# Optimization experiments

Hardware: AMD Instinct MI355X
Metric: run time of the kernel (lower is better)

The kernel has to match this reference:

```python
import jax, jax.numpy as jnp
from jax import lax
import numpy as np

OBS_DIM, POP_DIM, ACT_DIM, DE_POP = 256, 10, 8, 10
HID1, HID2 = 256, 256
SPIKE_TS = 25
ENC_VTH = 0.999
CDECAY = 0.5
VDECAY = 0.75
VTH_TEMPORAL = 0.5  # NEURON_VTH_*_temporal stays at its init value 0.5
GRAD_WIN = 0.5


@jax.custom_vjp
def enc_spike(v):
    return (v > ENC_VTH).astype(v.dtype)

def _es_fwd(v):
    return enc_spike(v), None

def _es_bwd(_, g):
    return (g,)  # straight-through

enc_spike.defvjp(_es_fwd, _es_bwd)


@jax.custom_vjp
def rect_spike(v, vth):
    return (v > vth).astype(v.dtype)

def _rs_fwd(v, vth):
    return rect_spike(v, vth), (v, vth)

def _rs_bwd(res, g):
    v, vth = res
    # rectangular pseudo-gradient window; vth is detached in the original (numpy roundtrip)
    return (g * (jnp.abs(v - vth) < GRAD_WIN).astype(g.dtype), jnp.zeros_like(vth))

rect_spike.defvjp(_rs_fwd, _rs_bwd)


def setup_inputs() -> dict:
    key = jax.random.key(0)
    ks = jax.random.split(key, 10)
    B = 2048
    obs = jax.random.normal(ks[0], (B, OBS_DIM), dtype=jnp.float32)
    # encoder Gaussian receptive-field params
    enc_mean = jnp.broadcast_to(jnp.linspace(-3.0, 3.0, POP_DIM, dtype=jnp.float32), (1, OBS_DIM, POP_DIM))
    enc_std = jnp.full((1, OBS_DIM, POP_DIM), 0.15, dtype=jnp.float32)
    n_in = OBS_DIM * POP_DIM
    out_pop = ACT_DIM * DE_POP
    w1 = jax.random.normal(ks[1], (HID1, n_in), dtype=jnp.float32) / np.sqrt(n_in)
    b1 = jnp.zeros((HID1,), dtype=jnp.float32)
    w2 = jax.random.normal(ks[2], (HID2, HID1), dtype=jnp.float32) / np.sqrt(HID1)
    b2 = jnp.zeros((HID2,), dtype=jnp.float32)
    w3 = jax.random.normal(ks[3], (out_pop, HID2), dtype=jnp.float32) / np.sqrt(HID2)
    b3 = jnp.zeros((out_pop,), dtype=jnp.float32)
    dec_w = jax.random.normal(ks[4], (ACT_DIM, DE_POP), dtype=jnp.float32) / np.sqrt(DE_POP)
    dec_b = jnp.zeros((ACT_DIM,), dtype=jnp.float32)
    return {"obs": obs, "enc_mean": enc_mean, "enc_std": enc_std,
            "w1": w1, "b1": b1, "w2": w2, "b2": b2, "w3": w3, "b3": b3,
            "dec_w": dec_w, "dec_b": dec_b, "batch_size": B}


def _forward(obs, enc_mean, enc_std, w1, b1, w2, b2, w3, b3, dec_w, dec_b):
    B = obs.shape[0]
    # --- population encoder: Gaussian receptive fields -> regular spike train ---
    pop_act = jnp.exp(-0.5 * (obs[:, :, None] - enc_mean) ** 2 / (enc_std ** 2))
    pop_act = pop_act.reshape(B, OBS_DIM * POP_DIM)  # [B, N]

    def enc_step(volt, _):
        volt = volt + pop_act
        s = enc_spike(volt)
        return volt - s * ENC_VTH, s

    _, in_spikes = lax.scan(enc_step, jnp.zeros_like(pop_act), None, length=SPIKE_TS)  # [T, B, N]

    # --- spike MLP with LIF neurons and dynamic threshold ---
    def lif_dth(x, W, b, state):
        c, v_prev, s = state
        c = c * CDECAY + x @ W.T + b
        v = v_prev * VDECAY * (1.0 - s) + c
        # dynamic threshold (detached in original via numpy roundtrip)
        vth = lax.stop_gradient(0.5 * VTH_TEMPORAL + 0.5 * (jnp.exp((v_prev - v) / 3.0) - 1.0))
        s = rect_spike(v, vth)
        return (c, v, s)

    def zeros_state(n):
        z = jnp.zeros((B, n), dtype=obs.dtype)
        return (z, z, z)

    init = (zeros_state(HID1), zeros_state(HID2), zeros_state(ACT_DIM * DE_POP))

    def mlp_step(states, x):
        s1 = lif_dth(x, w1, b1, states[0])
        s2 = lif_dth(s1[2], w2, b2, states[1])
        s3 = lif_dth(s2[2], w3, b3, states[2])
        return (s1, s2, s3), s3[2]

    _, out_spikes = lax.scan(mlp_step, init, in_spikes)  # [T, B, out_pop]
    pop_out = out_spikes.sum(axis=0) / SPIKE_TS  # rate decode

    # --- decoder: grouped Conv1d(kernel=pop_dim) == per-action dot product, then tanh ---
    raw = jnp.einsum('bap,ap->ba', pop_out.reshape(B, ACT_DIM, DE_POP), dec_w) + dec_b
    return jnp.tanh(raw)


def reference(obs, enc_mean, enc_std, w1, b1, w2, b2, w3, b3, dec_w, dec_b, batch_size):
    return _forward(obs, enc_mean, enc_std, w1, b1, w2, b2, w3, b3, dec_w, dec_b)
```

## Files before the change

### kernel.cpp

```cpp
#include <hip/hip_runtime.h>
#include <stdint.h>

#define NB 2048
#define OBSD 256
#define POP 10
#define NIN 2560
#define H 256
#define OUTP 80
#define TS 25
#define CAP 256

typedef __attribute__((ext_vector_type(2))) float f2;

__device__ __forceinline__ float exp_cr(float x) {
    return (float)exp((double)x);
}

__device__ __forceinline__ int rfl(int v) {
    return __builtin_amdgcn_readfirstlane(v);
}

struct Acc25 {
    f2 p[12];
    float last;
};

__device__ __forceinline__ void acc_zero(Acc25& a) {
    #pragma unroll
    for (int i = 0; i < 12; ++i) { a.p[i].x = 0.0f; a.p[i].y = 0.0f; }
    a.last = 0.0f;
}

__device__ __forceinline__ void acc_fold(Acc25& acc, Acc25& part) {
    #pragma unroll
    for (int i = 0; i < 12; ++i) {
        acc.p[i].x = __fadd_rn(acc.p[i].x, part.p[i].x);
        acc.p[i].y = __fadd_rn(acc.p[i].y, part.p[i].y);
        part.p[i].x = 0.0f; part.p[i].y = 0.0f;
    }
    acc.last = __fadd_rn(acc.last, part.last);
    part.last = 0.0f;
}

__device__ __forceinline__ void acc_unpack(const Acc25& a, float* __restrict__ t) {
    #pragma unroll
    for (int i = 0; i < 12; ++i) { t[2 * i] = a.p[i].x; t[2 * i + 1] = a.p[i].y; }
    t[24] = a.last;
}

__device__ __forceinline__ void fma25(float w, const float* __restrict__ rec, float lastv, Acc25& a) {
    f2 wp; wp.x = w; wp.y = w;
    float4 q[6];
    #pragma unroll
    for (int i = 0; i < 6; ++i) q[i] = ((const float4*)rec)[i];
    const f2* r2 = (const f2*)q;
    #pragma unroll
    for (int i = 0; i < 12; ++i) {
#if __has_builtin(__builtin_elementwise_fma)
        a.p[i] = __builtin_elementwise_fma(wp, r2[i], a.p[i]);
#else
        a.p[i].x = fmaf(w, r2[i].x, a.p[i].x);
        a.p[i].y = fmaf(w, r2[i].y, a.p[i].y);
#endif
    }
    a.last = fmaf(w, lastv, a.last);
}

__device__ __forceinline__ void write_rec(float* __restrict__ recs, float* __restrict__ rec24,
                                          int pos, uint32_t m) {
    if (pos >= CAP) return;
    float f[24];
    #pragma unroll
    for (int t = 0; t < 24; ++t) f[t] = (m >> t) & 1u ? 1.0f : 0.0f;
    float4* dst = (float4*)&recs[pos * 24];
    #pragma unroll
    for (int p = 0; p < 6; ++p)
        dst[p] = make_float4(f[4 * p], f[4 * p + 1], f[4 * p + 2], f[4 * p + 3]);
    rec24[pos] = (m >> 24) & 1u ? 1.0f : 0.0f;
}

template<bool FOLD>
__device__ __forceinline__ void walk(int n, const float* __restrict__ wt, int tid,
        const int* __restrict__ idxL, const float* __restrict__ recs,
        const float* __restrict__ rec24, Acc25& acc, Acc25& part, int& nextB)
{
    Acc25& tgt = FOLD ? part : acc;
    int pi0 = 0, pi1 = 0, pi2 = 0, pi3 = 0;
    float pw0 = 0, pw1 = 0, pw2 = 0, pw3 = 0;
    if (n > 0) { pi0 = rfl(idxL[0]); pw0 = wt[pi0 + tid]; }
    if (n > 1) { pi1 = rfl(idxL[1]); pw1 = wt[pi1 + tid]; }
    if (n > 2) { pi2 = rfl(idxL[2]); pw2 = wt[pi2 + tid]; }
    if (n > 3) { pi3 = rfl(idxL[3]); pw3 = wt[pi3 + tid]; }
    int j = 0;
    for (; j + 4 <= n; j += 4) {
        int ci0 = pi0, ci1 = pi1, ci2 = pi2, ci3 = pi3;
        float cw0 = pw0, cw1 = pw1, cw2 = pw2, cw3 = pw3;
        if (j + 4 < n) { pi0 = rfl(idxL[j + 4]); pw0 = wt[pi0 + tid]; }
        if (j + 5 < n) { pi1 = rfl(idxL[j + 5]); pw1 = wt[pi1 + tid]; }
        if (j + 6 < n) { pi2 = rfl(idxL[j + 6]); pw2 = wt[pi2 + tid]; }
        if (j + 7 < n) { pi3 = rfl(idxL[j + 7]); pw3 = wt[pi3 + tid]; }
        if (FOLD) { while (ci0 >= nextB) { acc_fold(acc, part); nextB += 320 * H; } }
        fma25(cw0, recs + j * 24, rec24[j], tgt);
        if (FOLD) { while (ci1 >= nextB) { acc_fold(acc, part); nextB += 320 * H; } }
        fma25(cw1, recs + (j + 1) * 24, rec24[j + 1], tgt);
        if (FOLD) { while (ci2 >= nextB) { acc_fold(acc, part); nextB += 320 * H; } }
        fma25(cw2, recs + (j + 2) * 24, rec24[j + 2], tgt);
        if (FOLD) { while (ci3 >= nextB) { acc_fold(acc, part); nextB += 320 * H; } }
        fma25(cw3, recs + (j + 3) * 24, rec24[j + 3], tgt);
    }
    for (; j < n; ++j) {
        int ii = rfl(idxL[j]);
        float wv = wt[ii + tid];
        if (FOLD) { while (ii >= nextB) { acc_fold(acc, part); nextB += 320 * H; } }
        fma25(wv, recs + j * 24, rec24[j], tgt);
    }
}

__global__ __launch_bounds__(256) void k0_transpose(
    const float* __restrict__ w1, const float* __restrict__ w2, const float* __restrict__ w3,
    float* __restrict__ w1t, float* __restrict__ w2t, float* __restrict__ w3t)
{
    __shared__ float tile[32][33];
    int bid = blockIdx.x;
    const float* src; float* dst; int R, C, tr, tc;
    if (bid < 640)      { src = w1; dst = w1t; R = 256; C = NIN; tr = bid / 80; tc = bid % 80; }
    else if (bid < 704) { int t = bid - 640; src = w2; dst = w2t; R = 256; C = 256; tr = t / 8; tc = t % 8; }
    else                { int t = bid - 704; src = w3; dst = w3t; R = OUTP; C = 256; tr = t / 8; tc = t % 8; }
    const int tx = threadIdx.x & 31, ty = threadIdx.x >> 5;
    const int r0 = tr * 32, c0 = tc * 32;
    #pragma unroll
    for (int i = 0; i < 4; ++i) {
        int r = r0 + ty + i * 8, c = c0 + tx;
        if (r < R && c < C) tile[ty + i * 8][tx] = src[r * C + c];
    }
    __syncthreads();
    #pragma unroll
    for (int i = 0; i < 4; ++i) {
        int c = c0 + ty + i * 8, r = r0 + tx;
        if (c < C && r < R) dst[c * R + r] = tile[tx][ty + i * 8];
    }
}

__device__ __forceinline__ void lif_step(float x, float bv, float& c, float& v, float& s) {
    float cn = __fadd_rn(__fadd_rn(__fmul_rn(c, 0.5f), x), bv);
    c = cn;
    float vp = v;
    float t  = __fmul_rn(__fmul_rn(vp, 0.75f), __fadd_rn(1.0f, -s));
    float vn = __fadd_rn(t, cn);
    float ag = __fdiv_rn(__fadd_rn(vp, -vn), 3.0f);
    v = vn;
    float ex_a  = __expf(ag);
    float vth_a = 0.25f + 0.5f * (ex_a - 1.0f);
    float delta = 1e-5f * (ex_a + fabsf(vth_a) + 1.0f);
    if (vn > vth_a + delta) {
        s = 1.0f;
    } else if (vn < vth_a - delta) {
        s = 0.0f;
    } else {
        float ex  = exp_cr(ag);
        float vth = __fadd_rn(0.25f, __fmul_rn(0.5f, __fadd_rn(ex, -1.0f)));
        s = (vn > vth) ? 1.0f : 0.0f;
    }
}

__global__ __launch_bounds__(256, 6) void k1_fused(
    const float* __restrict__ obs, const float* __restrict__ emean, const float* __restrict__ estd,
    const float* __restrict__ w1t, const float* __restrict__ w2t, const float* __restrict__ w3t,
    const float* __restrict__ b1, const float* __restrict__ b2, const float* __restrict__ b3,
    const float* __restrict__ dw, const float* __restrict__ db, float* __restrict__ out)
{
    __shared__ __align__(16) float recs[CAP * 24];
    __shared__ float rec24[CAP];
    __shared__ int   idxL[CAP];
    __shared__ uint32_t cntA[40];
    __shared__ uint32_t waveCnt[4];
    __shared__ float cnt3[OUTP];

    const int tid = threadIdx.x;
    const int wave = tid >> 6, lane = tid & 63;
    const int b = blockIdx.x;
    const unsigned long long below = (1ull << lane) - 1ull;

    uint32_t msk[10];
    #pragma unroll
    for (int k = 0; k < 10; ++k) {
        int i = k * 256 + tid;
        int o = i / 10;
        float x  = obs[b * OBSD + o];
        float mu = emean[i];
        float sd = estd[i];
        float d  = __fadd_rn(x, -mu);
        float d2 = __fmul_rn(d, d);
        float nm = __fmul_rn(-0.5f, d2);
        float dn = __fmul_rn(sd, sd);
        float arg = __fdiv_rn(nm, dn);
        uint32_t m = 0;
        if (arg >= -3.23f) {
            float a  = exp_cr(arg);
            float volt = 0.0f;
            #pragma unroll
            for (int t = 0; t < TS; ++t) {
                volt = __fadd_rn(volt, a);
                if (volt > 0.999f) { m |= (1u << t); volt = __fadd_rn(volt, -0.999f); }
            }
        }
        msk[k] = m;
    }

    #pragma unroll
    for (int k = 0; k < 10; ++k) {
        unsigned long long bal = __ballot(msk[k] != 0u);
        if (lane == 0) cntA[k * 4 + wave] = (uint32_t)__popcll(bal);
    }
    __syncthreads();

    Acc25 acc, part;
    acc_zero(acc); acc_zero(part);
    int nextB = 320 * H;
    int run = 0;
    #pragma unroll
    for (int k = 0; k < 10; ++k) {
        if (k == 5) {
            __syncthreads();
            walk<true>(run, w1t, tid, idxL, recs, rec24, acc, part, nextB);
            __syncthreads();
            run = 0;
        }
        int tot = 0, pre = 0;
        #pragma unroll
        for (int w = 0; w < 4; ++w) {
            int c = (int)cntA[k * 4 + w];
            tot += c;
            if (w < wave) pre += c;
        }
        uint32_t m = msk[k];
        unsigned long long bal = __ballot(m != 0u);
        if (m) {
            int pos = run + pre + (int)__popcll(bal & below);
            idxL[pos] = (k * 256 + tid) * H;
            write_rec(recs, rec24, pos, m);
        }
        run += tot;
    }
    __syncthreads();
    walk<true>(run, w1t, tid, idxL, recs, rec24, acc, part, nextB);
    acc_fold(acc, part);

    uint32_t m1 = 0;
    {
        float cur[TS];
        acc_unpack(acc, cur);
        const float b1v = b1[tid];
        float c1 = 0, v1 = 0, s1 = 0;
        #pragma unroll
        for (int t = 0; t < TS; ++t) {
            lif_step(cur[t], b1v, c1, v1, s1);
            if (s1 != 0.0f) m1 |= (1u << t);
        }
    }
    unsigned long long bal1 = __ballot(m1 != 0u);
    if (lane == 0) waveCnt[wave] = (uint32_t)__popcll(bal1);
    __syncthreads();
    int base1 = 0, n1 = 0;
    #pragma unroll
    for (int w = 0; w < 4; ++w) {
        if (w < wave) base1 += (int)waveCnt[w];
        n1 += (int)waveCnt[w];
    }
    if (m1) {
        int pos = base1 + (int)__popcll(bal1 & below);
        idxL[pos] = tid * H;
        write_rec(recs, rec24, pos, m1);
    }
    __syncthreads();

    Acc25 acc2;
    acc_zero(acc2);
    {
        int dummyB = 0x7fffffff;
        walk<false>(n1, w2t, tid, idxL, recs, rec24, acc2, acc2, dummyB);
    }
    uint32_t m2 = 0;
    {
        float cur[TS];
        acc_unpack(acc2, cur);
        const float b2v = b2[tid];
        float c2 = 0, v2 = 0, s2 = 0;
        #pragma unroll
        for (int t = 0; t < TS; ++t) {
            lif_step(cur[t], b2v, c2, v2, s2);
            if (s2 != 0.0f) m2 |= (1u << t);
        }
    }
    unsigned long long bal2 = __ballot(m2 != 0u);
    if (lane == 0) waveCnt[wave] = (uint32_t)__popcll(bal2);
    __syncthreads();
    int base2 = 0, n2 = 0;
    #pragma unroll
    for (int w = 0; w < 4; ++w) {
        if (w < wave) base2 += (int)waveCnt[w];
        n2 += (int)waveCnt[w];
    }
    if (m2) {
        int pos = base2 + (int)__popcll(bal2 & below);
        idxL[pos] = tid * OUTP;
        write_rec(recs, rec24, pos, m2);
    }
    __syncthreads();

    if (tid < OUTP) {
        Acc25 x3;
        acc_zero(x3);
        int dummyB = 0x7fffffff;
        walk<false>(n2, w3t, tid, idxL, recs, rec24, x3, x3, dummyB);
        float cur[TS];
        acc_unpack(x3, cur);
        const float b3v = b3[tid];
        float c3 = 0, v3 = 0, s3 = 0, ct = 0;
        #pragma unroll
        for (int t = 0; t < TS; ++t) {
            lif_step(cur[t], b3v, c3, v3, s3);
            ct += s3;
        }
        cnt3[tid] = ct;
    }
    __syncthreads();

    if (tid < 8) {
        float raw = 0.0f;
        #pragma unroll
        for (int pp = 0; pp < POP; ++pp) {
            float po = __fdiv_rn(cnt3[tid * POP + pp], 25.0f);
            raw = __fadd_rn(raw, __fmul_rn(po, dw[tid * POP + pp]));
        }
        raw = __fadd_rn(raw, db[tid]);
        out[b * 8 + tid] = (float)tanh((double)raw);
    }
}

extern "C" void kernel_launch(void* const* d_in, const int* in_sizes, int n_in,
                              void* d_out, int out_size, void* d_ws, size_t ws_size,
                              hipStream_t stream) {
    const float* obs   = (const float*)d_in[0];
    const float* emean = (const float*)d_in[1];
    const float* estd  = (const float*)d_in[2];
    const float* w1    = (const float*)d_in[3];
    const float* b1    = (const float*)d_in[4];
    const float* w2    = (const float*)d_in[5];
    const float* b2    = (const float*)d_in[6];
    const float* w3    = (const float*)d_in[7];
    const float* b3    = (const float*)d_in[8];
    const float* dw    = (const float*)d_in[9];
    const float* db    = (const float*)d_in[10];
    float* out = (float*)d_out;

    char* ws = (char*)d_ws;
    float* w1t = (float*)(ws);
    float* w2t = (float*)(ws + 2621440);
    float* w3t = (float*)(ws + 2883584);

    k0_transpose<<<728, 256, 0, stream>>>(w1, w2, w3, w1t, w2t, w3t);
    k1_fused<<<NB, 256, 0, stream>>>(obs, emean, estd, w1t, w2t, w3t,
                                     b1, b2, b3, dw, db, out);
}
```

Baseline: 383.0 us.

## Shrink shared spike buffer with chunked walks and raise occupancy target

Cuts the shared spike-record capacity from 256 to 88 entries and processes every layer's active inputs in chunks of that size, each chunk bracketed by block barriers. Per-thread spike masks move to shared memory and per-group bases are prefix-summed once. The launch bound is raised to 8 blocks per CU and the weight walk is unrolled by 2 instead of 4. All of this aims to lower LDS and register use so more blocks fit per CU. The LIF step also swaps the divide by 3 for a reciprocal multiply and widens the fallback tolerance. The cost is extra barriers and chunk loops, plus less memory-level parallelism in the gather.

```diff
diff --git a/kernel.cpp b/kernel.cpp
--- a/kernel.cpp
+++ b/kernel.cpp
@@ -8,7 +8,7 @@
 #define H 256
 #define OUTP 80
 #define TS 25
-#define CAP 256
+#define CAP 88
 
 typedef __attribute__((ext_vector_type(2))) float f2;
 
@@ -68,7 +68,6 @@
 
 __device__ __forceinline__ void write_rec(float* __restrict__ recs, float* __restrict__ rec24,
                                           int pos, uint32_t m) {
-    if (pos >= CAP) return;
     float f[24];
     #pragma unroll
     for (int t = 0; t < 24; ++t) f[t] = (m >> t) & 1u ? 1.0f : 0.0f;
@@ -79,42 +78,28 @@
     rec24[pos] = (m >> 24) & 1u ? 1.0f : 0.0f;
 }
 
-template<bool FOLD>
-__device__ __forceinline__ void walk(int n, const float* __restrict__ wt, int tid,
-        const int* __restrict__ idxL, const float* __restrict__ recs,
-        const float* __restrict__ rec24, Acc25& acc, Acc25& part, int& nextB)
-{
-    Acc25& tgt = FOLD ? part : acc;
-    int pi0 = 0, pi1 = 0, pi2 = 0, pi3 = 0;
-    float pw0 = 0, pw1 = 0, pw2 = 0, pw3 = 0;
-    if (n > 0) { pi0 = rfl(idxL[0]); pw0 = wt[pi0 + tid]; }
-    if (n > 1) { pi1 = rfl(idxL[1]); pw1 = wt[pi1 + tid]; }
-    if (n > 2) { pi2 = rfl(idxL[2]); pw2 = wt[pi2 + tid]; }
-    if (n > 3) { pi3 = rfl(idxL[3]); pw3 = wt[pi3 + tid]; }
-    int j = 0;
-    for (; j + 4 <= n; j += 4) {
-        int ci0 = pi0, ci1 = pi1, ci2 = pi2, ci3 = pi3;
-        float cw0 = pw0, cw1 = pw1, cw2 = pw2, cw3 = pw3;
-        if (j + 4 < n) { pi0 = rfl(idxL[j + 4]); pw0 = wt[pi0 + tid]; }
-        if (j + 5 < n) { pi1 = rfl(idxL[j + 5]); pw1 = wt[pi1 + tid]; }
-        if (j + 6 < n) { pi2 = rfl(idxL[j + 6]); pw2 = wt[pi2 + tid]; }
-        if (j + 7 < n) { pi3 = rfl(idxL[j + 7]); pw3 = wt[pi3 + tid]; }
-        if (FOLD) { while (ci0 >= nextB) { acc_fold(acc, part); nextB += 320 * H; } }
-        fma25(cw0, recs + j * 24, rec24[j], tgt);
-        if (FOLD) { while (ci1 >= nextB) { acc_fold(acc, part); nextB += 320 * H; } }
-        fma25(cw1, recs + (j + 1) * 24, rec24[j + 1], tgt);
-        if (FOLD) { while (ci2 >= nextB) { acc_fold(acc, part); nextB += 320 * H; } }
-        fma25(cw2, recs + (j + 2) * 24, rec24[j + 2], tgt);
-        if (FOLD) { while (ci3 >= nextB) { acc_fold(acc, part); nextB += 320 * H; } }
-        fma25(cw3, recs + (j + 3) * 24, rec24[j + 3], tgt);
-    }
-    for (; j < n; ++j) {
-        int ii = rfl(idxL[j]);
-        float wv = wt[ii + tid];
-        if (FOLD) { while (ii >= nextB) { acc_fold(acc, part); nextB += 320 * H; } }
-        fma25(wv, recs + j * 24, rec24[j], tgt);
-    }
-}
+#define WALK_BODY(CNT, WT, DOFOLD, TGT)                                     \
+  do {                                                                      \
+    int _n = (CNT);                                                         \
+    int _pi0 = 0, _pi1 = 0; float _pw0 = 0, _pw1 = 0;                       \
+    if (_n > 0) { _pi0 = rfl(idxL[0]); _pw0 = (WT)[_pi0 + tid]; }           \
+    if (_n > 1) { _pi1 = rfl(idxL[1]); _pw1 = (WT)[_pi1 + tid]; }           \
+    int _j = 0;                                                             \
+    for (; _j + 2 <= _n; _j += 2) {                                         \
+      int _c0 = _pi0, _c1 = _pi1; float _w0 = _pw0, _w1 = _pw1;             \
+      if (_j + 2 < _n) { _pi0 = rfl(idxL[_j + 2]); _pw0 = (WT)[_pi0 + tid]; } \
+      if (_j + 3 < _n) { _pi1 = rfl(idxL[_j + 3]); _pw1 = (WT)[_pi1 + tid]; } \
+      if (DOFOLD) { while (_c0 >= nextB) { acc_fold(acc, part); nextB += 320 * H; } } \
+      fma25(_w0, &recs[_j * 24], rec24[_j], TGT);                           \
+      if (DOFOLD) { while (_c1 >= nextB) { acc_fold(acc, part); nextB += 320 * H; } } \
+      fma25(_w1, &recs[(_j + 1) * 24], rec24[_j + 1], TGT);                 \
+    }                                                                       \
+    for (; _j < _n; ++_j) {                                                 \
+      int _ii = rfl(idxL[_j]); float _wv = (WT)[_ii + tid];                 \
+      if (DOFOLD) { while (_ii >= nextB) { acc_fold(acc, part); nextB += 320 * H; } } \
+      fma25(_wv, &recs[_j * 24], rec24[_j], TGT);                           \
+    }                                                                       \
+  } while (0)
 
 __global__ __launch_bounds__(256) void k0_transpose(
     const float* __restrict__ w1, const float* __restrict__ w2, const float* __restrict__ w3,
@@ -147,23 +132,25 @@
     float vp = v;
     float t  = __fmul_rn(__fmul_rn(vp, 0.75f), __fadd_rn(1.0f, -s));
     float vn = __fadd_rn(t, cn);
-    float ag = __fdiv_rn(__fadd_rn(vp, -vn), 3.0f);
+    float d  = __fadd_rn(vp, -vn);
     v = vn;
-    float ex_a  = __expf(ag);
+    float ag_f  = __fmul_rn(d, 0.33333334f);
+    float ex_a  = __expf(ag_f);
     float vth_a = 0.25f + 0.5f * (ex_a - 1.0f);
-    float delta = 1e-5f * (ex_a + fabsf(vth_a) + 1.0f);
+    float delta = (1e-5f + 1e-6f * fabsf(ag_f)) * (ex_a + fabsf(vth_a) + 1.0f);
     if (vn > vth_a + delta) {
         s = 1.0f;
     } else if (vn < vth_a - delta) {
         s = 0.0f;
     } else {
+        float ag  = __fdiv_rn(d, 3.0f);
         float ex  = exp_cr(ag);
         float vth = __fadd_rn(0.25f, __fmul_rn(0.5f, __fadd_rn(ex, -1.0f)));
         s = (vn > vth) ? 1.0f : 0.0f;
     }
 }
 
-__global__ __launch_bounds__(256, 6) void k1_fused(
+__global__ __launch_bounds__(256, 8) void k1_fused(
     const float* __restrict__ obs, const float* __restrict__ emean, const float* __restrict__ estd,
     const float* __restrict__ w1t, const float* __restrict__ w2t, const float* __restrict__ w3t,
     const float* __restrict__ b1, const float* __restrict__ b2, const float* __restrict__ b3,
@@ -172,7 +159,9 @@
     __shared__ __align__(16) float recs[CAP * 24];
     __shared__ float rec24[CAP];
     __shared__ int   idxL[CAP];
+    __shared__ uint32_t mskL[256 * 10];
     __shared__ uint32_t cntA[40];
+    __shared__ uint32_t gbase[11];
     __shared__ uint32_t waveCnt[4];
     __shared__ float cnt3[OUTP];
 
@@ -181,16 +170,14 @@
     const int b = blockIdx.x;
     const unsigned long long below = (1ull << lane) - 1ull;
 
-    uint32_t msk[10];
-    #pragma unroll
     for (int k = 0; k < 10; ++k) {
         int i = k * 256 + tid;
         int o = i / 10;
         float x  = obs[b * OBSD + o];
         float mu = emean[i];
         float sd = estd[i];
-        float d  = __fadd_rn(x, -mu);
-        float d2 = __fmul_rn(d, d);
+        float dd = __fadd_rn(x, -mu);
+        float d2 = __fmul_rn(dd, dd);
         float nm = __fmul_rn(-0.5f, d2);
         float dn = __fmul_rn(sd, sd);
         float arg = __fdiv_rn(nm, dn);
@@ -204,46 +191,52 @@
                 if (volt > 0.999f) { m |= (1u << t); volt = __fadd_rn(volt, -0.999f); }
             }
         }
-        msk[k] = m;
-    }
-
-    #pragma unroll
-    for (int k = 0; k < 10; ++k) {
-        unsigned long long bal = __ballot(msk[k] != 0u);
+        mskL[tid * 10 + k] = m;
+        unsigned long long bal = __ballot(m != 0u);
         if (lane == 0) cntA[k * 4 + wave] = (uint32_t)__popcll(bal);
     }
     __syncthreads();
+    if (tid == 0) {
+        uint32_t run = 0;
+        #pragma unroll
+        for (int k = 0; k < 10; ++k) {
+            gbase[k] = run;
+            run += cntA[k * 4] + cntA[k * 4 + 1] + cntA[k * 4 + 2] + cntA[k * 4 + 3];
+        }
+        gbase[10] = run;
+    }
+    __syncthreads();
+    const int nTot = (int)gbase[10];
 
     Acc25 acc, part;
     acc_zero(acc); acc_zero(part);
     int nextB = 320 * H;
-    int run = 0;
-    #pragma unroll
-    for (int k = 0; k < 10; ++k) {
-        if (k == 5) {
-            __syncthreads();
-            walk<true>(run, w1t, tid, idxL, recs, rec24, acc, part, nextB);
-            __syncthreads();
-            run = 0;
-        }
-        int tot = 0, pre = 0;
-        #pragma unroll
-        for (int w = 0; w < 4; ++w) {
-            int c = (int)cntA[k * 4 + w];
-            tot += c;
-            if (w < wave) pre += c;
-        }
-        uint32_t m = msk[k];
-        unsigned long long bal = __ballot(m != 0u);
-        if (m) {
-            int pos = run + pre + (int)__popcll(bal & below);
-            idxL[pos] = (k * 256 + tid) * H;
-            write_rec(recs, rec24, pos, m);
-        }
-        run += tot;
-    }
-    __syncthreads();
-    walk<true>(run, w1t, tid, idxL, recs, rec24, acc, part, nextB);
+
+    for (int start = 0; start < nTot; start += CAP) {
+        const int end = (nTot - start < CAP) ? nTot : start + CAP;
+        const int count = end - start;
+        #pragma unroll
+        for (int k = 0; k < 10; ++k) {
+            int gb = (int)gbase[k], ge = (int)gbase[k + 1];
+            if (ge <= start || gb >= end) continue;
+            uint32_t m = mskL[tid * 10 + k];
+            unsigned long long bal = __ballot(m != 0u);
+            if (m) {
+                int pre = 0;
+                #pragma unroll
+                for (int w = 0; w < 4; ++w) if (w < wave) pre += (int)cntA[k * 4 + w];
+                int pos = gb + pre + (int)__popcll(bal & below);
+                if (pos >= start && pos < end) {
+                    int slot = pos - start;
+                    idxL[slot] = (k * 256 + tid) * H;
+                    write_rec(recs, rec24, slot, m);
+                }
+            }
+        }
+        __syncthreads();
+        WALK_BODY(count, w1t, 1, part);
+        __syncthreads();
+    }
     acc_fold(acc, part);
 
     uint32_t m1 = 0;
@@ -267,18 +260,21 @@
         if (w < wave) base1 += (int)waveCnt[w];
         n1 += (int)waveCnt[w];
     }
-    if (m1) {
-        int pos = base1 + (int)__popcll(bal1 & below);
-        idxL[pos] = tid * H;
-        write_rec(recs, rec24, pos, m1);
-    }
-    __syncthreads();
+    const int pos1 = base1 + (int)__popcll(bal1 & below);
 
     Acc25 acc2;
     acc_zero(acc2);
-    {
-        int dummyB = 0x7fffffff;
-        walk<false>(n1, w2t, tid, idxL, recs, rec24, acc2, acc2, dummyB);
+    for (int start = 0; start < n1; start += CAP) {
+        const int end = (n1 - start < CAP) ? n1 : start + CAP;
+        const int count = end - start;
+        if (m1 && pos1 >= start && pos1 < end) {
+            int slot = pos1 - start;
+            idxL[slot] = tid * H;
+            write_rec(recs, rec24, slot, m1);
+        }
+        __syncthreads();
+        WALK_BODY(count, w2t, 0, acc2);
+        __syncthreads();
     }
     uint32_t m2 = 0;
     {
@@ -301,18 +297,25 @@
         if (w < wave) base2 += (int)waveCnt[w];
         n2 += (int)waveCnt[w];
     }
-    if (m2) {
-        int pos = base2 + (int)__popcll(bal2 & below);
-        idxL[pos] = tid * OUTP;
-        write_rec(recs, rec24, pos, m2);
-    }
-    __syncthreads();
-
+    const int pos2 = base2 + (int)__popcll(bal2 & below);
+
+    Acc25 x3;
+    acc_zero(x3);
+    for (int start = 0; start < n2; start += CAP) {
+        const int end = (n2 - start < CAP) ? n2 : start + CAP;
+        const int count = end - start;
+        if (m2 && pos2 >= start && pos2 < end) {
+            int slot = pos2 - start;
+            idxL[slot] = tid * OUTP;
+            write_rec(recs, rec24, slot, m2);
+        }
+        __syncthreads();
+        if (tid < OUTP) {
+            WALK_BODY(count, w3t, 0, x3);
+        }
+        __syncthreads();
+    }
     if (tid < OUTP) {
-        Acc25 x3;
-        acc_zero(x3);
-        int dummyB = 0x7fffffff;
-        walk<false>(n2, w3t, tid, idxL, recs, rec24, x3, x3, dummyB);
         float cur[TS];
         acc_unpack(x3, cur);
         const float b3v = b3[tid];
```

After: 500.3 us. 30.6% more time.
